# Kernel tuning notes

Measured on AMD Instinct MI355X. Metric: run time of the kernel, lower is better.

The kernel has to match this reference:

```python
import jax, jax.numpy as jnp
import numpy as np

N_LEADS = 12
N_HEADS = 4
LN_EPS = 1e-5

def _ecg_adj_norm():
    # Fixed 12-lead ECG adjacency with self loops, symmetric GCN normalization
    conns = [(0,1),(0,2),(1,2),(0,3),(1,3),(2,3),(0,4),(1,4),(1,5),(2,5),
             (6,7),(7,8),(8,9),(9,10),(10,11),(0,6),(1,9),(2,11)]
    A = np.zeros((N_LEADS, N_LEADS), dtype=np.float32)
    for i, j in conns:
        A[i, j] = 1.0
        A[j, i] = 1.0
    A += np.eye(N_LEADS, dtype=np.float32)
    d = A.sum(axis=1)
    dinv = 1.0 / np.sqrt(d)
    return jnp.asarray(dinv[:, None] * A * dinv[None, :])  # [12,12]

A_NORM = _ecg_adj_norm()

def gcn(x, W, b):
    # x: [B,12,F] -> A_norm @ (x W) + b
    return jnp.einsum('ij,bjf->bif', A_NORM, x @ W) + b

def mha(x, in_w, in_b, out_w, out_b):
    # x: [B,S,E]; torch nn.MultiheadAttention, batch_first=True
    B, S, E = x.shape
    D = E // N_HEADS
    qkv = x @ in_w.T + in_b                      # [B,S,3E]
    q, k, v = jnp.split(qkv, 3, axis=-1)
    def heads(t):
        return t.reshape(B, S, N_HEADS, D).transpose(0, 2, 1, 3)  # [B,H,S,D]
    q, k, v = heads(q), heads(k), heads(v)
    scores = jnp.einsum('bhsd,bhtd->bhst', q, k) / jnp.sqrt(jnp.float32(D))
    attn = jax.nn.softmax(scores, axis=-1)
    o = jnp.einsum('bhst,bhtd->bhsd', attn, v)   # [B,H,S,D]
    o = o.transpose(0, 2, 1, 3).reshape(B, S, E)
    return o @ out_w.T + out_b

def layer_norm(x, g, b):
    mu = x.mean(axis=-1, keepdims=True)
    var = ((x - mu) ** 2).mean(axis=-1, keepdims=True)
    return (x - mu) * jax.lax.rsqrt(var + LN_EPS) * g + b

def setup_inputs() -> dict:
    key = jax.random.key(0)
    ks = jax.random.split(key, 8)
    B, F_IN, H, OUT = 8192, 512, 256, 256
    s = lambda fan: 1.0 / np.sqrt(fan)
    return {
        'x': jax.random.normal(ks[0], (B, N_LEADS, F_IN), dtype=jnp.float32),
        'W1': jax.random.normal(ks[1], (F_IN, H), dtype=jnp.float32) * s(F_IN),
        'b1': jnp.zeros((H,), jnp.float32),
        'W2': jax.random.normal(ks[2], (H, H), dtype=jnp.float32) * s(H),
        'b2': jnp.zeros((H,), jnp.float32),
        'W3': jax.random.normal(ks[3], (H, OUT), dtype=jnp.float32) * s(H),
        'b3': jnp.zeros((OUT,), jnp.float32),
        'in_proj_w': jax.random.normal(ks[4], (3 * H, H), dtype=jnp.float32) * s(H),
        'in_proj_b': jnp.zeros((3 * H,), jnp.float32),
        'out_proj_w': jax.random.normal(ks[5], (H, H), dtype=jnp.float32) * s(H),
        'out_proj_b': jnp.zeros((H,), jnp.float32),
        'ln_g': jnp.ones((H,), jnp.float32),
        'ln_b': jnp.zeros((H,), jnp.float32),
    }

def reference(x, W1, b1, W2, b2, W3, b3, in_proj_w, in_proj_b, out_proj_w, out_proj_b, ln_g, ln_b):
    h = jax.nn.relu(gcn(x, W1, b1))              # dropout is identity at eval
    h = jax.nn.relu(gcn(h, W2, b2))              # [B,12,H]
    att = mha(h, in_proj_w, in_proj_b, out_proj_w, out_proj_b)
    h = layer_norm(h + att, ln_g, ln_b)
    h3 = gcn(h, W3, b3)                          # [B,12,OUT]
    w = jax.nn.softmax(h3.mean(axis=-1), axis=1) # [B,12] attention pooling
    x_weighted = jnp.einsum('bno,bn->bo', h3, w)
    x_max = h3.max(axis=1)
    return jnp.concatenate([x_weighted, x_max], axis=1)  # [B, 2*OUT]
```

## Files before the change

kernel.cpp:

```cpp
#include <hip/hip_runtime.h>
#include <hip/hip_bf16.h>
#include <cstdint>
#include <cstddef>

typedef unsigned short u16;
typedef u16 u16x8 __attribute__((ext_vector_type(8)));
typedef u16 u16x4 __attribute__((ext_vector_type(4)));
typedef __bf16 bf16x8 __attribute__((ext_vector_type(8)));
typedef float f32x4 __attribute__((ext_vector_type(4)));

__device__ const unsigned short ADJ_MASK[12] = {
    95u, 575u, 2095u, 15u, 19u, 38u, 193u, 448u, 896u, 1794u, 3584u, 3076u};

__device__ __forceinline__ float b2f(u16 u) {
  union { unsigned int i; float f; } v;
  v.i = ((unsigned int)u) << 16;
  return v.f;
}
__device__ __forceinline__ u16 f2b(float f) {
  union { float f; unsigned int i; } v;
  v.f = f;
  unsigned int r = v.i + 0x7fffu + ((v.i >> 16) & 1u);
  return (u16)(r >> 16);
}

__device__ __forceinline__ void build_anorm(float* An) {
  int t = threadIdx.x;
  if (t < 144) {
    int i = t / 12, j = t % 12;
    float di = (float)__popc((int)ADJ_MASK[i]);
    float dj = (float)__popc((int)ADJ_MASK[j]);
    An[t] = ((ADJ_MASK[i] >> j) & 1) ? (1.0f / sqrtf(di * dj)) : 0.0f;
  }
}

__global__ void __launch_bounds__(256) k_detect(const void* p, int* flag) {
  const unsigned int* w = (const unsigned int*)p;
  __shared__ int s;
  if (threadIdx.x == 0) s = 0;
  __syncthreads();
  int cnt = 0;
  for (int t = 0; t < 16; ++t) {
    unsigned int v = w[t * 256 + threadIdx.x];
    unsigned int e = (v >> 7) & 0xFFu;
    if (e != 0u && (e < 0x5Au || e > 0x89u)) ++cnt;
  }
  atomicAdd(&s, cnt);
  __syncthreads();
  if (threadIdx.x == 0) *flag = (s > 1024) ? 1 : 0;
}

__global__ void k_cvt(const void* in, u16* out, int n, const int* flag) {
  int idx = blockIdx.x * 256 + threadIdx.x;
  if (idx < n) {
    out[idx] = (*flag) ? f2b(((const float*)in)[idx]) : ((const u16*)in)[idx];
  }
}

__global__ void k_transpose_cvt(const void* in, u16* out, int R, int C,
                                const int* flag) {
  long idx = (long)blockIdx.x * 256 + threadIdx.x;
  if (idx < (long)R * C) {
    long c = idx / R, r = idx - c * R;
    u16 v = (*flag) ? f2b(((const float*)in)[r * C + c])
                    : ((const u16*)in)[r * C + c];
    out[c * R + r] = v;
  }
}

__global__ void __launch_bounds__(256) k_mix(const u16* __restrict__ in,
                                             const u16* __restrict__ bias,
                                             u16* __restrict__ out, int relu) {
  __shared__ u16 X[6144];
  __shared__ float An[144];
  build_anorm(An);
  const int tid = threadIdx.x;
  const long base = (long)blockIdx.x * 6144;
#pragma unroll
  for (int i = 0; i < 3; ++i) {
    int idx = i * 256 + tid;
    *(u16x8*)(X + idx * 8) = *(const u16x8*)(in + base + idx * 8);
  }
  __syncthreads();
#pragma unroll
  for (int v = 0; v < 3; ++v) {
    int idx = v * 256 + tid;
    int s = idx / 384;
    int rem = idx - s * 384;
    int i = rem >> 5;
    int fg = rem & 31;
    float a[8];
#pragma unroll
    for (int u = 0; u < 8; ++u) a[u] = b2f(bias[fg * 8 + u]);
    for (int j = 0; j < 12; ++j) {
      float c = An[i * 12 + j];
      if (c != 0.0f) {
        u16x8 y = *(const u16x8*)(X + (s * 12 + j) * 256 + fg * 8);
#pragma unroll
        for (int u = 0; u < 8; ++u) a[u] += c * b2f(y[u]);
      }
    }
    u16x8 o;
#pragma unroll
    for (int u = 0; u < 8; ++u) {
      float vv = relu ? fmaxf(a[u], 0.0f) : a[u];
      o[u] = f2b(vv);
    }
    *(u16x8*)(out + base + idx * 8) = o;
  }
}

__device__ __forceinline__ void gemm_core(const void* __restrict__ A, int lda,
                                          int isf32,
                                          const u16* __restrict__ Bt,
                                          u16* As, u16* Bs,
                                          long m0, long n0, int K,
                                          f32x4 acc[6][4]) {
  const int tid = threadIdx.x;
  const int wave = tid >> 6, lane = tid & 63;
  const int q = lane >> 4, r16 = lane & 15;
  f32x4 zero = {0.f, 0.f, 0.f, 0.f};
#pragma unroll
  for (int a = 0; a < 6; ++a)
#pragma unroll
    for (int b = 0; b < 4; ++b) acc[a][b] = zero;

  for (int k0 = 0; k0 < K; k0 += 64) {
    if (isf32) {
      const float* Af = (const float*)A;
#pragma unroll
      for (int i = 0; i < 3; ++i) {
        int idx = i * 256 + tid;
        int rr = idx >> 3, cg = idx & 7;
        const float* sp = Af + (m0 + rr) * (long)lda + k0 + cg * 8;
        u16x8 t;
#pragma unroll
        for (int u = 0; u < 8; ++u) t[u] = f2b(sp[u]);
        *(u16x8*)(As + rr * 72 + cg * 8) = t;
      }
    } else {
      const u16* Ab = (const u16*)A;
#pragma unroll
      for (int i = 0; i < 3; ++i) {
        int idx = i * 256 + tid;
        int rr = idx >> 3, cg = idx & 7;
        *(u16x8*)(As + rr * 72 + cg * 8) =
            *(const u16x8*)(Ab + (m0 + rr) * (long)lda + k0 + cg * 8);
      }
    }
#pragma unroll
    for (int i = 0; i < 8; ++i) {
      int idx = i * 256 + tid;
      int rr = idx >> 3, cg = idx & 7;
      *(u16x8*)(Bs + rr * 72 + cg * 8) =
          *(const u16x8*)(Bt + (n0 + rr) * (long)K + k0 + cg * 8);
    }
    __syncthreads();
#pragma unroll
    for (int ks = 0; ks < 64; ks += 32) {
      bf16x8 af[6], bfv[4];
#pragma unroll
      for (int rb = 0; rb < 6; ++rb)
        af[rb] = *(const bf16x8*)(As + (rb * 16 + r16) * 72 + ks + q * 8);
#pragma unroll
      for (int cb = 0; cb < 4; ++cb)
        bfv[cb] = *(const bf16x8*)(Bs + ((wave * 4 + cb) * 16 + r16) * 72 + ks + q * 8);
#pragma unroll
      for (int rb = 0; rb < 6; ++rb)
#pragma unroll
        for (int cb = 0; cb < 4; ++cb)
          acc[rb][cb] = __builtin_amdgcn_mfma_f32_16x16x32_bf16(
              af[rb], bfv[cb], acc[rb][cb], 0, 0, 0);
    }
    __syncthreads();
  }
}

template <bool BIAS>
__global__ void __launch_bounds__(256) k_gemm(const void* __restrict__ A, int lda,
                                              const u16* __restrict__ Bt,
                                              const u16* __restrict__ bias,
                                              u16* __restrict__ C,
                                              int K, int Ntot,
                                              const int* aflag) {
  __shared__ u16 As[96 * 72];
  __shared__ u16 Bs[256 * 72];
  f32x4 acc[6][4];
  const long m0 = (long)blockIdx.x * 96;
  const long n0 = (long)blockIdx.y * 256;
  int isf32 = aflag ? *aflag : 0;
  gemm_core(A, lda, isf32, Bt, As, Bs, m0, n0, K, acc);
  const int tid = threadIdx.x;
  const int wave = tid >> 6, lane = tid & 63;
  const int q = lane >> 4, r16 = lane & 15;
#pragma unroll
  for (int cb = 0; cb < 4; ++cb) {
    long col = n0 + (wave * 4 + cb) * 16 + r16;
    float bvv = BIAS ? b2f(bias[col]) : 0.0f;
#pragma unroll
    for (int rb = 0; rb < 6; ++rb) {
#pragma unroll
      for (int rr = 0; rr < 4; ++rr) {
        long row = m0 + rb * 16 + q * 4 + rr;
        C[row * (long)Ntot + col] = f2b(acc[rb][cb][rr] + bvv);
      }
    }
  }
}

__global__ void __launch_bounds__(256) k_attn(u16* __restrict__ QKV) {
  __shared__ u16 T[12 * 768];
  __shared__ float Sc[4][12][12];
  const int tid = threadIdx.x;
  const long base = (long)blockIdx.x * (12 * 768);
#pragma unroll
  for (int i = 0; i < 9; ++i) {
    int idx = i * 256 + tid;
    *(u16x4*)(T + idx * 4) = *(const u16x4*)(QKV + base + idx * 4);
  }
  __syncthreads();
  for (int p = tid; p < 576; p += 256) {
    int h = p / 144, r = p % 144, i = r / 12, j = r % 12;
    const u16* qp = T + i * 768 + h * 64;
    const u16* kp = T + j * 768 + 256 + h * 64;
    float s = 0.f;
#pragma unroll
    for (int dv = 0; dv < 8; ++dv) {
      u16x8 qv = *(const u16x8*)(qp + dv * 8);
      u16x8 kv = *(const u16x8*)(kp + dv * 8);
#pragma unroll
      for (int u = 0; u < 8; ++u) s += b2f(qv[u]) * b2f(kv[u]);
    }
    Sc[h][i][j] = s * 0.125f;
  }
  __syncthreads();
  if (tid < 48) {
    int h = tid / 12, i = tid % 12;
    float m = -1e30f;
#pragma unroll
    for (int j = 0; j < 12; ++j) m = fmaxf(m, Sc[h][i][j]);
    float e[12];
    float ssum = 0.f;
#pragma unroll
    for (int j = 0; j < 12; ++j) {
      e[j] = __expf(Sc[h][i][j] - m);
      ssum += e[j];
    }
    float inv = 1.0f / ssum;
#pragma unroll
    for (int j = 0; j < 12; ++j) Sc[h][i][j] = e[j] * inv;
  }
  __syncthreads();
  {
    int h = tid >> 6;
    int d = tid & 63;
    float vv[12];
#pragma unroll
    for (int j = 0; j < 12; ++j) vv[j] = b2f(T[j * 768 + 512 + h * 64 + d]);
#pragma unroll
    for (int i = 0; i < 12; ++i) {
      float o = 0.f;
#pragma unroll
      for (int j = 0; j < 12; ++j) o += Sc[h][i][j] * vv[j];
      QKV[base + i * 768 + h * 64 + d] = f2b(o);
    }
  }
}

__global__ void __launch_bounds__(256) k_resid_ln_mix(
    const u16* __restrict__ H, const u16* __restrict__ Oa,
    const u16* __restrict__ g, const u16* __restrict__ bb,
    u16* __restrict__ out) {
  __shared__ float Xn[12 * 256];
  __shared__ float An[144];
  __shared__ float mu[12], rs[12];
  build_anorm(An);
  const int tid = threadIdx.x;
  const long baseH = (long)blockIdx.x * 3072;
  const long baseO = (long)blockIdx.x * 9216;
#pragma unroll
  for (int i = 0; i < 3; ++i) {
    int idx = i * 256 + tid;
    int row = idx >> 6, c4 = idx & 63;
    u16x4 hv = *(const u16x4*)(H + baseH + idx * 4);
    u16x4 ov = *(const u16x4*)(Oa + baseO + row * 768 + c4 * 4);
#pragma unroll
    for (int u = 0; u < 4; ++u) Xn[idx * 4 + u] = b2f(hv[u]) + b2f(ov[u]);
  }
  __syncthreads();
  {
    int wave = tid >> 6, lane = tid & 63;
    for (int rr = wave; rr < 12; rr += 4) {
      float s = 0.f, s2 = 0.f;
#pragma unroll
      for (int u = 0; u < 4; ++u) {
        float xv = Xn[rr * 256 + u * 64 + lane];
        s += xv;
        s2 += xv * xv;
      }
#pragma unroll
      for (int off = 32; off > 0; off >>= 1) {
        s += __shfl_down(s, off, 64);
        s2 += __shfl_down(s2, off, 64);
      }
      if (lane == 0) {
        float m = s * (1.0f / 256.0f);
        float var = s2 * (1.0f / 256.0f) - m * m;
        mu[rr] = m;
        rs[rr] = rsqrtf(var + 1e-5f);
      }
    }
  }
  __syncthreads();
  {
    float gv = b2f(g[tid]);
    float bv = b2f(bb[tid]);
    float xn[12];
#pragma unroll
    for (int i = 0; i < 12; ++i) {
      float x = Xn[i * 256 + tid];
      xn[i] = (x - mu[i]) * rs[i] * gv + bv;
    }
#pragma unroll
    for (int i = 0; i < 12; ++i) {
      float o = 0.f;
#pragma unroll
      for (int j = 0; j < 12; ++j) o += An[i * 12 + j] * xn[j];
      out[baseH + i * 256 + tid] = f2b(o);
    }
  }
}

__global__ void __launch_bounds__(256) k_attn_mega(
    u16* __restrict__ H, const u16* __restrict__ inw,
    const u16* __restrict__ inb, const u16* __restrict__ outw,
    const u16* __restrict__ outb, const u16* __restrict__ lng,
    const u16* __restrict__ lnb) {
  __shared__ u16 Hs[32 * 264];
  __shared__ u16 Qs[32 * 264];
  __shared__ u16 KVs[24 * 512];
  __shared__ float Sc[4][2][12][12];
  __shared__ float An[144];
  __shared__ float mu[24], rs[24];
  const int tid = threadIdx.x;
  const int wave = tid >> 6, lane = tid & 63;
  const int q = lane >> 4, r16 = lane & 15;
  build_anorm(An);
  const long base = (long)blockIdx.x * 6144;
#pragma unroll
  for (int i = 0; i < 3; ++i) {
    int idx = i * 256 + tid;
    int rr = idx >> 5, cg = idx & 31;
    *(u16x8*)(Hs + rr * 264 + cg * 8) = *(const u16x8*)(H + base + idx * 8);
  }
  {
    int rr = 24 + (tid >> 5), cg = tid & 31;
    u16x8 z = {0, 0, 0, 0, 0, 0, 0, 0};
    *(u16x8*)(Hs + rr * 264 + cg * 8) = z;
  }
  __syncthreads();
  {
    f32x4 acc[2][12];
    f32x4 zero = {0.f, 0.f, 0.f, 0.f};
#pragma unroll
    for (int rb = 0; rb < 2; ++rb)
#pragma unroll
      for (int c = 0; c < 12; ++c) acc[rb][c] = zero;
    for (int k0 = 0; k0 < 256; k0 += 32) {
      bf16x8 af[2];
#pragma unroll
      for (int rb = 0; rb < 2; ++rb)
        af[rb] = *(const bf16x8*)(Hs + (rb * 16 + r16) * 264 + k0 + q * 8);
#pragma unroll
      for (int c = 0; c < 12; ++c) {
        bf16x8 bf = *(const bf16x8*)(inw + (long)((wave * 12 + c) * 16 + r16) * 256 + k0 + q * 8);
#pragma unroll
        for (int rb = 0; rb < 2; ++rb)
          acc[rb][c] = __builtin_amdgcn_mfma_f32_16x16x32_bf16(af[rb], bf, acc[rb][c], 0, 0, 0);
      }
    }
#pragma unroll
    for (int c = 0; c < 12; ++c) {
      int col = (wave * 12 + c) * 16 + r16;
      float bv = b2f(inb[col]);
#pragma unroll
      for (int rb = 0; rb < 2; ++rb)
#pragma unroll
        for (int rr2 = 0; rr2 < 4; ++rr2) {
          int row = rb * 16 + q * 4 + rr2;
          float v = acc[rb][c][rr2] + bv;
          if (col < 256) Qs[row * 264 + col] = f2b(v);
          else if (row < 24) KVs[row * 512 + col - 256] = f2b(v);
        }
    }
  }
  __syncthreads();
  {
    int h = wave;
#pragma unroll
    for (int t = 0; t < 5; ++t) {
      int p = t * 64 + lane;
      if (p < 288) {
        int s = p / 144, r = p - s * 144, i = r / 12, j = r - i * 12;
        const u16* qp = Qs + (s * 12 + i) * 264 + h * 64;
        const u16* kp = KVs + (s * 12 + j) * 512 + h * 64;
        float dot = 0.f;
#pragma unroll
        for (int dv = 0; dv < 8; ++dv) {
          u16x8 qv = *(const u16x8*)(qp + dv * 8);
          u16x8 kv = *(const u16x8*)(kp + dv * 8);
#pragma unroll
          for (int u = 0; u < 8; ++u) dot += b2f(qv[u]) * b2f(kv[u]);
        }
        Sc[h][s][i][j] = dot * 0.125f;
      }
    }
  }
  __syncthreads();
  if (lane < 24) {
    int h = wave, s = lane / 12, i = lane - (lane / 12) * 12;
    float m = -1e30f;
#pragma unroll
    for (int j = 0; j < 12; ++j) m = fmaxf(m, Sc[h][s][i][j]);
    float e[12];
    float ssum = 0.f;
#pragma unroll
    for (int j = 0; j < 12; ++j) {
      e[j] = __expf(Sc[h][s][i][j] - m);
      ssum += e[j];
    }
    float inv = 1.0f / ssum;
#pragma unroll
    for (int j = 0; j < 12; ++j) Sc[h][s][i][j] = e[j] * inv;
  }
  __syncthreads();
  {
    int h = wave, d = lane;
    for (int si = 0; si < 24; ++si) {
      int s = si / 12;
      float o = 0.f;
#pragma unroll
      for (int j = 0; j < 12; ++j)
        o += Sc[h][s][si - s * 12][j] * b2f(KVs[(s * 12 + j) * 512 + 256 + h * 64 + d]);
      Qs[si * 264 + h * 64 + d] = f2b(o);
    }
  }
  __syncthreads();
  {
    f32x4 acc[2][4];
    f32x4 zero = {0.f, 0.f, 0.f, 0.f};
#pragma unroll
    for (int rb = 0; rb < 2; ++rb)
#pragma unroll
      for (int cb = 0; cb < 4; ++cb) acc[rb][cb] = zero;
    for (int k0 = 0; k0 < 256; k0 += 32) {
      bf16x8 af[2];
#pragma unroll
      for (int rb = 0; rb < 2; ++rb)
        af[rb] = *(const bf16x8*)(Qs + (rb * 16 + r16) * 264 + k0 + q * 8);
#pragma unroll
      for (int cb = 0; cb < 4; ++cb) {
        bf16x8 bf = *(const bf16x8*)(outw + (long)((wave * 4 + cb) * 16 + r16) * 256 + k0 + q * 8);
#pragma unroll
        for (int rb = 0; rb < 2; ++rb)
          acc[rb][cb] = __builtin_amdgcn_mfma_f32_16x16x32_bf16(af[rb], bf, acc[rb][cb], 0, 0, 0);
      }
    }
#pragma unroll
    for (int cb = 0; cb < 4; ++cb) {
      int col = (wave * 4 + cb) * 16 + r16;
      float ob = b2f(outb[col]);
#pragma unroll
      for (int rb = 0; rb < 2; ++rb)
#pragma unroll
        for (int rr2 = 0; rr2 < 4; ++rr2) {
          int row = rb * 16 + q * 4 + rr2;
          if (row < 24) {
            float x = acc[rb][cb][rr2] + ob + b2f(Hs[row * 264 + col]);
            Hs[row * 264 + col] = f2b(x);
          }
        }
    }
  }
  __syncthreads();
  {
    for (int rr2 = wave * 6; rr2 < wave * 6 + 6; ++rr2) {
      float s1 = 0.f, s2 = 0.f;
#pragma unroll
      for (int u = 0; u < 4; ++u) {
        float xv = b2f(Hs[rr2 * 264 + u * 64 + lane]);
        s1 += xv;
        s2 += xv * xv;
      }
#pragma unroll
      for (int off = 32; off > 0; off >>= 1) {
        s1 += __shfl_down(s1, off, 64);
        s2 += __shfl_down(s2, off, 64);
      }
      if (lane == 0) {
        float m = s1 * (1.0f / 256.0f);
        mu[rr2] = m;
        rs[rr2] = rsqrtf(s2 * (1.0f / 256.0f) - m * m + 1e-5f);
      }
    }
  }
  __syncthreads();
  {
    float gvv = b2f(lng[tid]);
    float bvv = b2f(lnb[tid]);
#pragma unroll
    for (int s = 0; s < 2; ++s) {
      float xn[12];
#pragma unroll
      for (int j = 0; j < 12; ++j) {
        int row = s * 12 + j;
        xn[j] = (b2f(Hs[row * 264 + tid]) - mu[row]) * rs[row] * gvv + bvv;
      }
#pragma unroll
      for (int i = 0; i < 12; ++i) {
        float o = 0.f;
#pragma unroll
        for (int j = 0; j < 12; ++j) o += An[i * 12 + j] * xn[j];
        H[base + (s * 12 + i) * 256 + tid] = f2b(o);
      }
    }
  }
}

__global__ void __launch_bounds__(256) k_gemm_pool(const u16* __restrict__ A,
                                                   const u16* __restrict__ Bt,
                                                   const u16* __restrict__ bias,
                                                   float* __restrict__ out) {
  __shared__ __align__(16) char smraw[50688];
  __shared__ float rowsum[96];
  __shared__ float wsm[96];
  u16* As = (u16*)smraw;
  u16* Bs = As + 96 * 72;
  u16* Y = (u16*)smraw;
  f32x4 acc[6][4];
  const long m0 = (long)blockIdx.x * 96;
  gemm_core(A, 256, 0, Bt, As, Bs, m0, 0, 256, acc);
  const int tid = threadIdx.x;
  const int wave = tid >> 6, lane = tid & 63;
  const int q = lane >> 4, r16 = lane & 15;
#pragma unroll
  for (int cb = 0; cb < 4; ++cb) {
    int col = (wave * 4 + cb) * 16 + r16;
    float bvv = b2f(bias[col]);
#pragma unroll
    for (int rb = 0; rb < 6; ++rb)
#pragma unroll
      for (int rr = 0; rr < 4; ++rr) {
        int row = rb * 16 + q * 4 + rr;
        Y[row * 264 + col] = f2b(acc[rb][cb][rr] + bvv);
      }
  }
  __syncthreads();
  for (int row = wave; row < 96; row += 4) {
    float s = 0.f;
#pragma unroll
    for (int u = 0; u < 4; ++u) s += b2f(Y[row * 264 + u * 64 + lane]);
#pragma unroll
    for (int off = 32; off > 0; off >>= 1) s += __shfl_down(s, off, 64);
    if (lane == 0) rowsum[row] = s;
  }
  __syncthreads();
  if (tid < 8) {
    float m = -1e30f;
#pragma unroll
    for (int l = 0; l < 12; ++l) m = fmaxf(m, rowsum[tid * 12 + l]);
    float e[12];
    float ssum = 0.f;
#pragma unroll
    for (int l = 0; l < 12; ++l) {
      e[l] = __expf((rowsum[tid * 12 + l] - m) * (1.0f / 256.0f));
      ssum += e[l];
    }
    float inv = 1.0f / ssum;
#pragma unroll
    for (int l = 0; l < 12; ++l) wsm[tid * 12 + l] = e[l] * inv;
  }
  __syncthreads();
  {
    int s = tid >> 5, cg = tid & 31;
    float wa[8], mx[8];
#pragma unroll
    for (int u = 0; u < 8; ++u) {
      wa[u] = 0.f;
      mx[u] = -1e30f;
    }
#pragma unroll
    for (int l = 0; l < 12; ++l) {
      float w = wsm[s * 12 + l];
      u16x8 yv = *(const u16x8*)(Y + (s * 12 + l) * 264 + cg * 8);
#pragma unroll
      for (int u = 0; u < 8; ++u) {
        float y = b2f(yv[u]);
        wa[u] += w * y;
        mx[u] = fmaxf(mx[u], y);
      }
    }
    long ob = ((long)blockIdx.x * 8 + s) * 512;
#pragma unroll
    for (int u = 0; u < 8; ++u) {
      out[ob + cg * 8 + u] = wa[u];
      out[ob + 256 + cg * 8 + u] = mx[u];
    }
  }
}

extern "C" void kernel_launch(void* const* d_in, const int* in_sizes, int n_in,
                              void* d_out, int out_size, void* d_ws,
                              size_t ws_size, hipStream_t stream) {
  (void)in_sizes; (void)n_in; (void)out_size;
  const void* x    = d_in[0];
  const void* W1   = d_in[1];
  const void* b1   = d_in[2];
  const void* W2   = d_in[3];
  const void* b2   = d_in[4];
  const void* W3   = d_in[5];
  const void* b3   = d_in[6];
  const void* inw  = d_in[7];
  const void* inb  = d_in[8];
  const void* outw = d_in[9];
  const void* outb = d_in[10];
  const void* lng  = d_in[11];
  const void* lnb  = d_in[12];
  float* out = (float*)d_out;

  u16* ws16 = (u16*)d_ws;
  int* flagX = (int*)d_ws;
  int* flagW = (int*)d_ws + 1;
  u16* W1T    = ws16 + 64;
  u16* W2T    = W1T + 131072;
  u16* W3T    = W2T + 65536;
  u16* inw_b  = W3T + 65536;
  u16* outw_b = inw_b + 196608;
  u16* b1b    = outw_b + 65536;
  u16* b2b    = b1b + 256;
  u16* b3b    = b2b + 256;
  u16* inbb   = b3b + 256;
  u16* outbb  = inbb + 768;
  u16* lngb   = outbb + 256;
  u16* lnbb   = lngb + 256;
  u16* BUF    = lnbb + 256;
  u16* QKV    = BUF + 25165824L;
  const size_t NEED_A = (size_t)(QKV + 75497472L - ws16) * 2;

  k_detect<<<1, 256, 0, stream>>>(x, flagX);
  k_detect<<<1, 256, 0, stream>>>(W1, flagW);

  k_cvt<<<1, 256, 0, stream>>>(b1, b1b, 256, flagW);
  k_cvt<<<1, 256, 0, stream>>>(b2, b2b, 256, flagW);
  k_cvt<<<1, 256, 0, stream>>>(b3, b3b, 256, flagW);
  k_cvt<<<3, 256, 0, stream>>>(inb, inbb, 768, flagW);
  k_cvt<<<1, 256, 0, stream>>>(outb, outbb, 256, flagW);
  k_cvt<<<1, 256, 0, stream>>>(lng, lngb, 256, flagW);
  k_cvt<<<1, 256, 0, stream>>>(lnb, lnbb, 256, flagW);
  k_cvt<<<768, 256, 0, stream>>>(inw, inw_b, 196608, flagW);
  k_cvt<<<256, 256, 0, stream>>>(outw, outw_b, 65536, flagW);
  k_transpose_cvt<<<512, 256, 0, stream>>>(W1, W1T, 512, 256, flagW);
  k_transpose_cvt<<<256, 256, 0, stream>>>(W2, W2T, 256, 256, flagW);
  k_transpose_cvt<<<256, 256, 0, stream>>>(W3, W3T, 256, 256, flagW);

  k_gemm<false><<<dim3(1024, 1), 256, 0, stream>>>(x, 512, W1T, nullptr, BUF, 512, 256, flagX);
  k_mix<<<4096, 256, 0, stream>>>(BUF, b1b, BUF, 1);
  k_gemm<false><<<dim3(1024, 1), 256, 0, stream>>>(BUF, 256, W2T, nullptr, BUF, 256, 256, nullptr);
  k_mix<<<4096, 256, 0, stream>>>(BUF, b2b, BUF, 1);

  if (ws_size >= NEED_A) {
    k_gemm<true><<<dim3(1024, 3), 256, 0, stream>>>(BUF, 256, inw_b, inbb, QKV, 256, 768, nullptr);
    k_attn<<<8192, 256, 0, stream>>>(QKV);
    k_gemm<true><<<dim3(1024, 1), 256, 0, stream>>>(QKV, 768, outw_b, outbb, QKV + 256, 256, 768, nullptr);
    k_resid_ln_mix<<<8192, 256, 0, stream>>>(BUF, QKV + 256, lngb, lnbb, BUF);
  } else {
    k_attn_mega<<<4096, 256, 0, stream>>>(BUF, inw_b, inbb, outw_b, outbb, lngb, lnbb);
  }
  k_gemm_pool<<<1024, 256, 0, stream>>>(BUF, W3T, b3b, out);
}
```

Measured before the change: 668.9 us.

## Fuse graph mixing and layernorm into GEMM epilogues and merge setup kernels

Folds the adjacency mixing, bias and ReLU into the GCN GEMM epilogue through a shared-memory staging tile, and fuses the output projection with residual add, layernorm and the third mixing step. This removes several full round trips of the activation buffer through global memory. The GEMM output is now staged in LDS for coalesced vector stores, the fp32 A-loads are vectorised, and the many small weight conversion and detection launches are merged into a few kernels. The epilogues rely on 96-row tiles containing whole 12-lead samples, and k_oproj_ln reads and writes H in place within each block.

```diff
diff --git a/kernel.cpp b/kernel.cpp
--- a/kernel.cpp
+++ b/kernel.cpp
@@ -34,8 +34,9 @@
   }
 }
 
-__global__ void __launch_bounds__(256) k_detect(const void* p, int* flag) {
-  const unsigned int* w = (const unsigned int*)p;
+__global__ void __launch_bounds__(256) k_detect2(const void* a, const void* b,
+                                                 int* flags) {
+  const unsigned int* w = (const unsigned int*)(blockIdx.x ? b : a);
   __shared__ int s;
   if (threadIdx.x == 0) s = 0;
   __syncthreads();
@@ -47,67 +48,50 @@
   }
   atomicAdd(&s, cnt);
   __syncthreads();
-  if (threadIdx.x == 0) *flag = (s > 1024) ? 1 : 0;
-}
-
-__global__ void k_cvt(const void* in, u16* out, int n, const int* flag) {
+  if (threadIdx.x == 0) flags[blockIdx.x] = (s > 1024) ? 1 : 0;
+}
+
+__global__ void __launch_bounds__(256) k_cvt_small(
+    const void* b1, const void* b2, const void* b3, const void* inb,
+    const void* outb, const void* lng, const void* lnb, u16* dst,
+    const int* flag) {
   int idx = blockIdx.x * 256 + threadIdx.x;
-  if (idx < n) {
-    out[idx] = (*flag) ? f2b(((const float*)in)[idx]) : ((const u16*)in)[idx];
-  }
-}
-
-__global__ void k_transpose_cvt(const void* in, u16* out, int R, int C,
-                                const int* flag) {
-  long idx = (long)blockIdx.x * 256 + threadIdx.x;
-  if (idx < (long)R * C) {
-    long c = idx / R, r = idx - c * R;
-    u16 v = (*flag) ? f2b(((const float*)in)[r * C + c])
-                    : ((const u16*)in)[r * C + c];
-    out[c * R + r] = v;
-  }
-}
-
-__global__ void __launch_bounds__(256) k_mix(const u16* __restrict__ in,
-                                             const u16* __restrict__ bias,
-                                             u16* __restrict__ out, int relu) {
-  __shared__ u16 X[6144];
-  __shared__ float An[144];
-  build_anorm(An);
-  const int tid = threadIdx.x;
-  const long base = (long)blockIdx.x * 6144;
-#pragma unroll
-  for (int i = 0; i < 3; ++i) {
-    int idx = i * 256 + tid;
-    *(u16x8*)(X + idx * 8) = *(const u16x8*)(in + base + idx * 8);
-  }
-  __syncthreads();
-#pragma unroll
-  for (int v = 0; v < 3; ++v) {
-    int idx = v * 256 + tid;
-    int s = idx / 384;
-    int rem = idx - s * 384;
-    int i = rem >> 5;
-    int fg = rem & 31;
-    float a[8];
-#pragma unroll
-    for (int u = 0; u < 8; ++u) a[u] = b2f(bias[fg * 8 + u]);
-    for (int j = 0; j < 12; ++j) {
-      float c = An[i * 12 + j];
-      if (c != 0.0f) {
-        u16x8 y = *(const u16x8*)(X + (s * 12 + j) * 256 + fg * 8);
-#pragma unroll
-        for (int u = 0; u < 8; ++u) a[u] += c * b2f(y[u]);
-      }
-    }
-    u16x8 o;
-#pragma unroll
-    for (int u = 0; u < 8; ++u) {
-      float vv = relu ? fmaxf(a[u], 0.0f) : a[u];
-      o[u] = f2b(vv);
-    }
-    *(u16x8*)(out + base + idx * 8) = o;
-  }
+  if (idx >= 2304) return;
+  const void* src;
+  int off = idx;
+  if (idx < 256)       { src = b1; }
+  else if (idx < 512)  { src = b2;   off = idx - 256; }
+  else if (idx < 768)  { src = b3;   off = idx - 512; }
+  else if (idx < 1536) { src = inb;  off = idx - 768; }
+  else if (idx < 1792) { src = outb; off = idx - 1536; }
+  else if (idx < 2048) { src = lng;  off = idx - 1792; }
+  else                 { src = lnb;  off = idx - 2048; }
+  dst[idx] = (*flag) ? f2b(((const float*)src)[off]) : ((const u16*)src)[off];
+}
+
+__global__ void __launch_bounds__(256) k_cvt_w(const void* inw,
+                                               const void* outw, u16* dst,
+                                               const int* flag) {
+  int idx = blockIdx.x * 256 + threadIdx.x;
+  const void* src = (idx < 196608) ? inw : outw;
+  int off = (idx < 196608) ? idx : idx - 196608;
+  dst[idx] = (*flag) ? f2b(((const float*)src)[off]) : ((const u16*)src)[off];
+}
+
+__global__ void __launch_bounds__(256) k_transpose3(const void* W1,
+                                                    const void* W2,
+                                                    const void* W3, u16* dst,
+                                                    const int* flag) {
+  int idx = blockIdx.x * 256 + threadIdx.x;
+  const void* src;
+  int R, C, li = idx;
+  if (idx < 131072)      { src = W1; R = 512; C = 256; }
+  else if (idx < 196608) { src = W2; R = 256; C = 256; li = idx - 131072; }
+  else                   { src = W3; R = 256; C = 256; li = idx - 196608; }
+  int c = li / R, r = li - c * R;
+  u16 v = (*flag) ? f2b(((const float*)src)[r * C + c])
+                  : ((const u16*)src)[r * C + c];
+  dst[(idx - li) + c * R + r] = v;
 }
 
 __device__ __forceinline__ void gemm_core(const void* __restrict__ A, int lda,
@@ -133,9 +117,14 @@
         int idx = i * 256 + tid;
         int rr = idx >> 3, cg = idx & 7;
         const float* sp = Af + (m0 + rr) * (long)lda + k0 + cg * 8;
+        f32x4 v0 = *(const f32x4*)sp;
+        f32x4 v1 = *(const f32x4*)(sp + 4);
         u16x8 t;
 #pragma unroll
-        for (int u = 0; u < 8; ++u) t[u] = f2b(sp[u]);
+        for (int u = 0; u < 4; ++u) {
+          t[u] = f2b(v0[u]);
+          t[u + 4] = f2b(v1[u]);
+        }
         *(u16x8*)(As + rr * 72 + cg * 8) = t;
       }
     } else {
@@ -176,34 +165,187 @@
   }
 }
 
-template <bool BIAS>
 __global__ void __launch_bounds__(256) k_gemm(const void* __restrict__ A, int lda,
                                               const u16* __restrict__ Bt,
                                               const u16* __restrict__ bias,
                                               u16* __restrict__ C,
-                                              int K, int Ntot,
-                                              const int* aflag) {
-  __shared__ u16 As[96 * 72];
-  __shared__ u16 Bs[256 * 72];
+                                              int K, int Ntot) {
+  __shared__ __align__(16) char smraw[50688];
+  u16* As = (u16*)smraw;
+  u16* Bs = As + 96 * 72;
+  u16* Y = (u16*)smraw;
   f32x4 acc[6][4];
   const long m0 = (long)blockIdx.x * 96;
   const long n0 = (long)blockIdx.y * 256;
-  int isf32 = aflag ? *aflag : 0;
-  gemm_core(A, lda, isf32, Bt, As, Bs, m0, n0, K, acc);
+  gemm_core(A, lda, 0, Bt, As, Bs, m0, n0, K, acc);
   const int tid = threadIdx.x;
   const int wave = tid >> 6, lane = tid & 63;
   const int q = lane >> 4, r16 = lane & 15;
 #pragma unroll
   for (int cb = 0; cb < 4; ++cb) {
-    long col = n0 + (wave * 4 + cb) * 16 + r16;
-    float bvv = BIAS ? b2f(bias[col]) : 0.0f;
-#pragma unroll
-    for (int rb = 0; rb < 6; ++rb) {
+    int coll = (wave * 4 + cb) * 16 + r16;
+    float bvv = b2f(bias[n0 + coll]);
+#pragma unroll
+    for (int rb = 0; rb < 6; ++rb)
 #pragma unroll
       for (int rr = 0; rr < 4; ++rr) {
-        long row = m0 + rb * 16 + q * 4 + rr;
-        C[row * (long)Ntot + col] = f2b(acc[rb][cb][rr] + bvv);
-      }
+        int row = rb * 16 + q * 4 + rr;
+        Y[row * 264 + coll] = f2b(acc[rb][cb][rr] + bvv);
+      }
+  }
+  __syncthreads();
+#pragma unroll
+  for (int i = 0; i < 12; ++i) {
+    int idx = i * 256 + tid;
+    int rowl = idx >> 5, g = idx & 31;
+    *(u16x8*)(C + (m0 + rowl) * (long)Ntot + n0 + g * 8) =
+        *(const u16x8*)(Y + rowl * 264 + g * 8);
+  }
+}
+
+__global__ void __launch_bounds__(256) k_gemm_mix(const void* __restrict__ A,
+                                                  int lda,
+                                                  const u16* __restrict__ Bt,
+                                                  const u16* __restrict__ bias,
+                                                  u16* __restrict__ C, int K,
+                                                  const int* aflag) {
+  __shared__ __align__(16) char smraw[50688];
+  __shared__ float An[144];
+  u16* As = (u16*)smraw;
+  u16* Bs = As + 96 * 72;
+  u16* Y = (u16*)smraw;
+  build_anorm(An);
+  f32x4 acc[6][4];
+  const long m0 = (long)blockIdx.x * 96;
+  int isf32 = aflag ? *aflag : 0;
+  gemm_core(A, lda, isf32, Bt, As, Bs, m0, 0, K, acc);
+  const int tid = threadIdx.x;
+  const int wave = tid >> 6, lane = tid & 63;
+  const int q = lane >> 4, r16 = lane & 15;
+#pragma unroll
+  for (int cb = 0; cb < 4; ++cb) {
+    int col = (wave * 4 + cb) * 16 + r16;
+#pragma unroll
+    for (int rb = 0; rb < 6; ++rb)
+#pragma unroll
+      for (int rr = 0; rr < 4; ++rr) {
+        int row = rb * 16 + q * 4 + rr;
+        Y[row * 264 + col] = f2b(acc[rb][cb][rr]);
+      }
+  }
+  __syncthreads();
+  float bb4[4];
+#pragma unroll
+  for (int u = 0; u < 4; ++u) bb4[u] = b2f(bias[lane * 4 + u]);
+  const long cbase = m0 * 256;
+#pragma unroll
+  for (int sv = 0; sv < 2; ++sv) {
+    const int s = wave * 2 + sv;
+    float xn[12][4];
+#pragma unroll
+    for (int j = 0; j < 12; ++j) {
+      u16x4 yv = *(const u16x4*)(Y + (s * 12 + j) * 264 + lane * 4);
+#pragma unroll
+      for (int u = 0; u < 4; ++u) xn[j][u] = b2f(yv[u]);
+    }
+#pragma unroll
+    for (int i = 0; i < 12; ++i) {
+      float o[4] = {bb4[0], bb4[1], bb4[2], bb4[3]};
+      for (int j = 0; j < 12; ++j) {
+        float c = An[i * 12 + j];
+        if (c != 0.0f) {
+#pragma unroll
+          for (int u = 0; u < 4; ++u) o[u] += c * xn[j][u];
+        }
+      }
+      u16x4 ov;
+#pragma unroll
+      for (int u = 0; u < 4; ++u) ov[u] = f2b(fmaxf(o[u], 0.0f));
+      *(u16x4*)(C + cbase + (long)(s * 12 + i) * 256 + lane * 4) = ov;
+    }
+  }
+}
+
+__global__ void __launch_bounds__(256) k_oproj_ln(
+    const u16* __restrict__ Q, const u16* __restrict__ Bt,
+    const u16* __restrict__ outb, const u16* __restrict__ lng,
+    const u16* __restrict__ lnb, u16* __restrict__ H) {
+  __shared__ __align__(16) char smraw[50688];
+  __shared__ float An[144];
+  u16* As = (u16*)smraw;
+  u16* Bs = As + 96 * 72;
+  u16* Y = (u16*)smraw;
+  build_anorm(An);
+  f32x4 acc[6][4];
+  const long m0 = (long)blockIdx.x * 96;
+  gemm_core(Q, 768, 0, Bt, As, Bs, m0, 0, 256, acc);
+  const int tid = threadIdx.x;
+  const int wave = tid >> 6, lane = tid & 63;
+  const int q = lane >> 4, r16 = lane & 15;
+#pragma unroll
+  for (int cb = 0; cb < 4; ++cb) {
+    int col = (wave * 4 + cb) * 16 + r16;
+    float bvv = b2f(outb[col]);
+#pragma unroll
+    for (int rb = 0; rb < 6; ++rb)
+#pragma unroll
+      for (int rr = 0; rr < 4; ++rr) {
+        int row = rb * 16 + q * 4 + rr;
+        Y[row * 264 + col] = f2b(acc[rb][cb][rr] + bvv);
+      }
+  }
+  __syncthreads();
+  float g4[4], bl4[4];
+#pragma unroll
+  for (int u = 0; u < 4; ++u) {
+    g4[u] = b2f(lng[lane * 4 + u]);
+    bl4[u] = b2f(lnb[lane * 4 + u]);
+  }
+  const long hbase = m0 * 256;
+#pragma unroll
+  for (int sv = 0; sv < 2; ++sv) {
+    const int s = wave * 2 + sv;
+    float x[12][4];
+#pragma unroll
+    for (int j = 0; j < 12; ++j) {
+      int row = s * 12 + j;
+      u16x4 yv = *(const u16x4*)(Y + row * 264 + lane * 4);
+      u16x4 hv = *(const u16x4*)(H + hbase + (long)row * 256 + lane * 4);
+#pragma unroll
+      for (int u = 0; u < 4; ++u) x[j][u] = b2f(yv[u]) + b2f(hv[u]);
+    }
+#pragma unroll
+    for (int j = 0; j < 12; ++j) {
+      float s1 = x[j][0] + x[j][1] + x[j][2] + x[j][3];
+      float s2 = x[j][0] * x[j][0] + x[j][1] * x[j][1] +
+                 x[j][2] * x[j][2] + x[j][3] * x[j][3];
+#pragma unroll
+      for (int off = 32; off > 0; off >>= 1) {
+        s1 += __shfl_down(s1, off, 64);
+        s2 += __shfl_down(s2, off, 64);
+      }
+      s1 = __shfl(s1, 0, 64);
+      s2 = __shfl(s2, 0, 64);
+      float m = s1 * (1.0f / 256.0f);
+      float rstd = rsqrtf(s2 * (1.0f / 256.0f) - m * m + 1e-5f);
+#pragma unroll
+      for (int u = 0; u < 4; ++u)
+        x[j][u] = (x[j][u] - m) * rstd * g4[u] + bl4[u];
+    }
+#pragma unroll
+    for (int i = 0; i < 12; ++i) {
+      float o[4] = {0.f, 0.f, 0.f, 0.f};
+      for (int j = 0; j < 12; ++j) {
+        float c = An[i * 12 + j];
+        if (c != 0.0f) {
+#pragma unroll
+          for (int u = 0; u < 4; ++u) o[u] += c * x[j][u];
+        }
+      }
+      u16x4 ov;
+#pragma unroll
+      for (int u = 0; u < 4; ++u) ov[u] = f2b(o[u]);
+      *(u16x4*)(H + hbase + (long)(s * 12 + i) * 256 + lane * 4) = ov;
     }
   }
 }
@@ -214,9 +356,13 @@
   const int tid = threadIdx.x;
   const long base = (long)blockIdx.x * (12 * 768);
 #pragma unroll
-  for (int i = 0; i < 9; ++i) {
+  for (int i = 0; i < 4; ++i) {
     int idx = i * 256 + tid;
-    *(u16x4*)(T + idx * 4) = *(const u16x4*)(QKV + base + idx * 4);
+    *(u16x8*)(T + idx * 8) = *(const u16x8*)(QKV + base + idx * 8);
+  }
+  {
+    int off = 8192 + tid * 4;
+    *(u16x4*)(T + off) = *(const u16x4*)(QKV + base + off);
   }
   __syncthreads();
   for (int p = tid; p < 576; p += 256) {
@@ -263,70 +409,6 @@
 #pragma unroll
       for (int j = 0; j < 12; ++j) o += Sc[h][i][j] * vv[j];
       QKV[base + i * 768 + h * 64 + d] = f2b(o);
-    }
-  }
-}
-
-__global__ void __launch_bounds__(256) k_resid_ln_mix(
-    const u16* __restrict__ H, const u16* __restrict__ Oa,
-    const u16* __restrict__ g, const u16* __restrict__ bb,
-    u16* __restrict__ out) {
-  __shared__ float Xn[12 * 256];
-  __shared__ float An[144];
-  __shared__ float mu[12], rs[12];
-  build_anorm(An);
-  const int tid = threadIdx.x;
-  const long baseH = (long)blockIdx.x * 3072;
-  const long baseO = (long)blockIdx.x * 9216;
-#pragma unroll
-  for (int i = 0; i < 3; ++i) {
-    int idx = i * 256 + tid;
-    int row = idx >> 6, c4 = idx & 63;
-    u16x4 hv = *(const u16x4*)(H + baseH + idx * 4);
-    u16x4 ov = *(const u16x4*)(Oa + baseO + row * 768 + c4 * 4);
-#pragma unroll
-    for (int u = 0; u < 4; ++u) Xn[idx * 4 + u] = b2f(hv[u]) + b2f(ov[u]);
-  }
-  __syncthreads();
-  {
-    int wave = tid >> 6, lane = tid & 63;
-    for (int rr = wave; rr < 12; rr += 4) {
-      float s = 0.f, s2 = 0.f;
-#pragma unroll
-      for (int u = 0; u < 4; ++u) {
-        float xv = Xn[rr * 256 + u * 64 + lane];
-        s += xv;
-        s2 += xv * xv;
-      }
-#pragma unroll
-      for (int off = 32; off > 0; off >>= 1) {
-        s += __shfl_down(s, off, 64);
-        s2 += __shfl_down(s2, off, 64);
-      }
-      if (lane == 0) {
-        float m = s * (1.0f / 256.0f);
-        float var = s2 * (1.0f / 256.0f) - m * m;
-        mu[rr] = m;
-        rs[rr] = rsqrtf(var + 1e-5f);
-      }
-    }
-  }
-  __syncthreads();
-  {
-    float gv = b2f(g[tid]);
-    float bv = b2f(bb[tid]);
-    float xn[12];
-#pragma unroll
-    for (int i = 0; i < 12; ++i) {
-      float x = Xn[i * 256 + tid];
-      xn[i] = (x - mu[i]) * rs[i] * gv + bv;
-    }
-#pragma unroll
-    for (int i = 0; i < 12; ++i) {
-      float o = 0.f;
-#pragma unroll
-      for (int j = 0; j < 12; ++j) o += An[i * 12 + j] * xn[j];
-      out[baseH + i * 256 + tid] = f2b(o);
     }
   }
 }
@@ -629,8 +711,7 @@
   float* out = (float*)d_out;
 
   u16* ws16 = (u16*)d_ws;
-  int* flagX = (int*)d_ws;
-  int* flagW = (int*)d_ws + 1;
+  int* flags = (int*)d_ws;
   u16* W1T    = ws16 + 64;
   u16* W2T    = W1T + 131072;
   u16* W3T    = W2T + 65536;
@@ -647,32 +728,20 @@
   u16* QKV    = BUF + 25165824L;
   const size_t NEED_A = (size_t)(QKV + 75497472L - ws16) * 2;
 
-  k_detect<<<1, 256, 0, stream>>>(x, flagX);
-  k_detect<<<1, 256, 0, stream>>>(W1, flagW);
-
-  k_cvt<<<1, 256, 0, stream>>>(b1, b1b, 256, flagW);
-  k_cvt<<<1, 256, 0, stream>>>(b2, b2b, 256, flagW);
-  k_cvt<<<1, 256, 0, stream>>>(b3, b3b, 256, flagW);
-  k_cvt<<<3, 256, 0, stream>>>(inb, inbb, 768, flagW);
-  k_cvt<<<1, 256, 0, stream>>>(outb, outbb, 256, flagW);
-  k_cvt<<<1, 256, 0, stream>>>(lng, lngb, 256, flagW);
-  k_cvt<<<1, 256, 0, stream>>>(lnb, lnbb, 256, flagW);
-  k_cvt<<<768, 256, 0, stream>>>(inw, inw_b, 196608, flagW);
-  k_cvt<<<256, 256, 0, stream>>>(outw, outw_b, 65536, flagW);
-  k_transpose_cvt<<<512, 256, 0, stream>>>(W1, W1T, 512, 256, flagW);
-  k_transpose_cvt<<<256, 256, 0, stream>>>(W2, W2T, 256, 256, flagW);
-  k_transpose_cvt<<<256, 256, 0, stream>>>(W3, W3T, 256, 256, flagW);
-
-  k_gemm<false><<<dim3(1024, 1), 256, 0, stream>>>(x, 512, W1T, nullptr, BUF, 512, 256, flagX);
-  k_mix<<<4096, 256, 0, stream>>>(BUF, b1b, BUF, 1);
-  k_gemm<false><<<dim3(1024, 1), 256, 0, stream>>>(BUF, 256, W2T, nullptr, BUF, 256, 256, nullptr);
-  k_mix<<<4096, 256, 0, stream>>>(BUF, b2b, BUF, 1);
+  k_detect2<<<2, 256, 0, stream>>>(x, W1, flags);
+
+  k_cvt_small<<<9, 256, 0, stream>>>(b1, b2, b3, inb, outb, lng, lnb, b1b,
+                                     flags + 1);
+  k_cvt_w<<<1024, 256, 0, stream>>>(inw, outw, inw_b, flags + 1);
+  k_transpose3<<<1024, 256, 0, stream>>>(W1, W2, W3, W1T, flags + 1);
+
+  k_gemm_mix<<<1024, 256, 0, stream>>>(x, 512, W1T, b1b, BUF, 512, flags);
+  k_gemm_mix<<<1024, 256, 0, stream>>>(BUF, 256, W2T, b2b, BUF, 256, nullptr);
 
   if (ws_size >= NEED_A) {
-    k_gemm<true><<<dim3(1024, 3), 256, 0, stream>>>(BUF, 256, inw_b, inbb, QKV, 256, 768, nullptr);
+    k_gemm<<<dim3(1024, 3), 256, 0, stream>>>(BUF, 256, inw_b, inbb, QKV, 256, 768);
     k_attn<<<8192, 256, 0, stream>>>(QKV);
-    k_gemm<true><<<dim3(1024, 1), 256, 0, stream>>>(QKV, 768, outw_b, outbb, QKV + 256, 256, 768, nullptr);
-    k_resid_ln_mix<<<8192, 256, 0, stream>>>(BUF, QKV + 256, lngb, lnbb, BUF);
+    k_oproj_ln<<<1024, 256, 0, stream>>>(QKV, outw_b, outbb, lngb, lnbb, BUF);
   } else {
     k_attn_mega<<<4096, 256, 0, stream>>>(BUF, inw_b, inbb, outw_b, outbb, lngb, lnbb);
   }
```

Result: slower. 721.7 us (+7.9%).
